# Optimization experiments

Measured on AMD Instinct MI355X. Metric: run time of the kernel, lower is better.

The kernel has to match this reference:

```python
import jax, jax.numpy as jnp
import numpy as np

ALPHA = 0.0005
BETA = 0.1
MARGIN = 100.0
GCN_WEIGHT = 0.1
EPS = 1e-8


def _bce(pred, tgt):
    # torch.nn.BCELoss with mean reduction (pred already in (0,1))
    return -jnp.mean(tgt * jnp.log(pred) + (1.0 - tgt) * jnp.log(1.0 - pred))


def _gcn_loss(nodes, labels, sample_idx):
    # nodes: [B, M, D], labels: [B, M] in {-1,0,1}, sample_idx: [B, S]
    n2 = jnp.sum(nodes * nodes, axis=-1)                               # [B, M]
    s_nodes = jnp.take_along_axis(nodes, sample_idx[:, :, None], axis=1)  # [B, S, D]
    s_lab = jnp.take_along_axis(labels, sample_idx, axis=1)            # [B, S]
    s2 = jnp.take_along_axis(n2, sample_idx, axis=1)                   # [B, S]
    cross = jnp.einsum('bsd,bmd->bsm', s_nodes, nodes)                 # [B, S, M]
    d2 = jnp.maximum(s2[:, :, None] + n2[:, None, :] - 2.0 * cross, 0.0)
    valid = labels >= 0
    same = (labels[:, None, :] == s_lab[:, :, None]) & valid[:, None, :]
    opp = (labels[:, None, :] != s_lab[:, :, None]) & valid[:, None, :]
    BIG = jnp.float32(1e30)
    # farthest same-label node, closest opposite-label node (L2 distance; sqrt is monotone)
    pos_idx = jnp.argmax(jnp.where(same, d2, -BIG), axis=-1)           # [B, S]
    neg_idx = jnp.argmin(jnp.where(opp, d2, BIG), axis=-1)             # [B, S]
    s_norm = jnp.sqrt(s2)

    def _cos(idx):
        dot = jnp.take_along_axis(cross, idx[:, :, None], axis=2)[..., 0]
        nb = jnp.sqrt(jnp.take_along_axis(n2, idx, axis=1))
        return dot / (jnp.maximum(s_norm, EPS) * jnp.maximum(nb, EPS))

    pos_loss = jnp.where(jnp.any(same, axis=-1), _cos(pos_idx), 0.0)
    neg_loss = jnp.where(jnp.any(opp, axis=-1), _cos(neg_idx), 0.0)
    return jnp.sum(pos_loss + neg_loss)


def setup_inputs() -> dict:
    key = jax.random.key(0)
    ks = jax.random.split(key, 10)
    B, T, D, C, M, S = 32, 750, 2048, 20, 750, 64
    score_act = jax.random.uniform(ks[0], (B, C)) * 0.98 + 0.01   # sigmoid-like probs in (0,1)
    score_bkg = jax.random.uniform(ks[1], (B, C)) * 0.98 + 0.01
    feat_act = jax.random.normal(ks[2], (B, T, D))
    feat_bkg = jax.random.normal(ks[3], (B, T, D))
    label = (jax.random.uniform(ks[4], (B, C)) < 0.3).astype(jnp.float32)
    label = label.at[:, 0].set(1.0)  # guarantee >=1 positive class per video
    gt = jax.random.uniform(ks[5], (B, T, C))
    cas = jax.random.normal(ks[6], (B, T, C))
    nodes = jax.random.normal(ks[7], (B, M, D))
    nodes_label = jax.random.randint(ks[8], (B, M), 0, 2)
    sample_idx = jax.random.randint(ks[9], (B, S), 0, M)
    return {'score_act': score_act, 'score_bkg': score_bkg, 'feat_act': feat_act,
            'feat_bkg': feat_bkg, 'label': label, 'gt': gt, 'cas': cas,
            'nodes': nodes, 'nodes_label': nodes_label, 'sample_idx': sample_idx}


def reference(score_act, score_bkg, feat_act, feat_bkg, label, gt, cas, nodes, nodes_label, sample_idx):
    label_n = label / jnp.sum(label, axis=1, keepdims=True)
    loss_cls = _bce(score_act, label_n)
    label_bkg = jnp.ones_like(label) / label.shape[1]
    loss_be = _bce(score_bkg, label_bkg)
    loss_act = jnp.maximum(MARGIN - jnp.linalg.norm(jnp.mean(feat_act, axis=1), axis=1), 0.0)
    loss_bkg = jnp.linalg.norm(jnp.mean(feat_bkg, axis=1), axis=1)
    loss_um = jnp.mean((loss_act + loss_bkg) ** 2)
    loss_gcn = GCN_WEIGHT * _gcn_loss(nodes, nodes_label, sample_idx)
    return loss_cls + ALPHA * loss_um + BETA * loss_be + loss_gcn
```

## Files before the change

kernel.cpp:

```cpp
#include <hip/hip_runtime.h>
#include <math.h>

#define BB 32
#define TT 750
#define DD 2048
#define CC 20
#define MM 750
#define SS 64
#define MT 64
#define NT 12
#define TSPLIT 8
#define TCH 94

#define GCN_BLOCKS (NT * BB)
#define FEAT_BLOCKS (2 * BB * TSPLIT * 2)
#define TOT_BLOCKS (GCN_BLOCKS + FEAT_BLOCKS + 1)

#define ALPHA_W 0.0005f
#define BETA_W 0.1f
#define MARGIN_W 100.0f
#define GCN_W 0.1f
#define EPS_V 1e-8f

#define WS_LOSS01 0
#define WS_N2ACT 16
#define WS_N2BKG 48
#define WS_GCNB 80
#define WS_S2 128
#define WS_CAND 4096
#define WS_COLSUM 200704

typedef __attribute__((ext_vector_type(8))) short bf16x8;
typedef __attribute__((ext_vector_type(4))) float f32x4;

__device__ __forceinline__ unsigned short f2bf(float f) {
  unsigned int u = __float_as_uint(f);
  return (unsigned short)((u + 0x7FFFu + ((u >> 16) & 1u)) >> 16);
}

__global__ __launch_bounds__(256, 3) void mega_kernel(
    const float* __restrict__ score_act, const float* __restrict__ score_bkg,
    const float* __restrict__ feat_act, const float* __restrict__ feat_bkg,
    const float* __restrict__ label, const float* __restrict__ nodes,
    const int* __restrict__ nlab, const int* __restrict__ sidx,
    float* __restrict__ ws) {
  int bx = blockIdx.x;
  int tid = threadIdx.x;
  int q11 = bx / 11, r11 = bx % 11;

  if (bx < TOT_BLOCKS - 1 && r11 < 3) {
    int idx = q11 * 3 + r11;
    int b = idx / NT, tile = idx % NT;

    __shared__ __align__(16) unsigned short sAh[64 * 64];
    __shared__ __align__(16) unsigned short sBh[64 * 64];
    __shared__ float sS2[SS];
    __shared__ float sN2[MT];
    __shared__ int sSlab[SS];
    __shared__ int sMlab[MT];

    if (tid < SS) {
      sSlab[tid] = nlab[b * MM + sidx[b * SS + tid]];
    } else if (tid < SS + MT) {
      int ml = tid - SS;
      int m = tile * MT + ml;
      sMlab[ml] = (m < MM) ? nlab[b * MM + m] : -2;
    }

    int r = tid >> 2, p = tid & 3;
    const float* aRow = nodes + ((size_t)b * MM + sidx[b * SS + r]) * DD;
    int mrow = tile * MT + r;
    bool bval = (mrow < MM);
    const float* bRow = nodes + ((size_t)b * MM + (bval ? mrow : 0)) * DD;

    int wslot[4];
#pragma unroll
    for (int j = 0; j < 4; ++j) {
      int u = p + 4 * j;
      wslot[j] = r * 64 + ((((u >> 1) ^ (r & 7)) << 1) + (u & 1)) * 4;
    }

    int lane = tid & 63, w = tid >> 6;
    int g = lane >> 4, c = lane & 15;

    float aSq = 0.f, bSq = 0.f;
    f32x4 acc[4];
#pragma unroll
    for (int f = 0; f < 4; ++f) acc[f] = (f32x4){0.f, 0.f, 0.f, 0.f};

    float4 pa[4], pb[4];
#pragma unroll
    for (int j = 0; j < 4; ++j) {
      int off = (p + 4 * j) * 4;
      pa[j] = *(const float4*)(aRow + off);
      pb[j] = *(const float4*)(bRow + off);
    }

    for (int ch = 0; ch < 32; ++ch) {
      __syncthreads();
#pragma unroll
      for (int j = 0; j < 4; ++j) {
        float4 v = pa[j];
        aSq += v.x * v.x + v.y * v.y + v.z * v.z + v.w * v.w;
        unsigned int lo = (unsigned int)f2bf(v.x) | ((unsigned int)f2bf(v.y) << 16);
        unsigned int hi = (unsigned int)f2bf(v.z) | ((unsigned int)f2bf(v.w) << 16);
        *(uint2*)&sAh[wslot[j]] = make_uint2(lo, hi);
        float4 t = pb[j];
        bSq += t.x * t.x + t.y * t.y + t.z * t.z + t.w * t.w;
        lo = (unsigned int)f2bf(t.x) | ((unsigned int)f2bf(t.y) << 16);
        hi = (unsigned int)f2bf(t.z) | ((unsigned int)f2bf(t.w) << 16);
        *(uint2*)&sBh[wslot[j]] = make_uint2(lo, hi);
      }
      __syncthreads();
      if (ch < 31) {
        const float* ap = aRow + (ch + 1) * 64;
        const float* bp = bRow + (ch + 1) * 64;
#pragma unroll
        for (int j = 0; j < 4; ++j) {
          int off = (p + 4 * j) * 4;
          pa[j] = *(const float4*)(ap + off);
          pb[j] = *(const float4*)(bp + off);
        }
      }
#pragma unroll
      for (int kk = 0; kk < 2; ++kk) {
        int su = kk * 4 + g;
        int arow = w * 16 + c;
        bf16x8 af = *(const bf16x8*)&sAh[arow * 64 + (su ^ (arow & 7)) * 8];
#pragma unroll
        for (int f = 0; f < 4; ++f) {
          int brow = f * 16 + c;
          bf16x8 bfr = *(const bf16x8*)&sBh[brow * 64 + (su ^ (brow & 7)) * 8];
          acc[f] = __builtin_amdgcn_mfma_f32_16x16x32_bf16(af, bfr, acc[f], 0, 0, 0);
        }
      }
    }

    aSq += __shfl_down(aSq, 2, 4);
    aSq += __shfl_down(aSq, 1, 4);
    bSq += __shfl_down(bSq, 2, 4);
    bSq += __shfl_down(bSq, 1, 4);
    if (p == 0) {
      sS2[r] = aSq;
      sN2[r] = bSq;
    }
    __syncthreads();

    if (tile == 0 && tid < SS) ws[WS_S2 + b * SS + tid] = sS2[tid];

#pragma unroll
    for (int reg = 0; reg < 4; ++reg) {
      int s = w * 16 + g * 4 + reg;
      int slab = sSlab[s];
      float s2v = sS2[s];
      float posD = -3.4e38f, posC = 0.f, posN = 0.f;
      int posI = -1;
      float negD = 3.4e38f, negC = 0.f, negN = 0.f;
      int negI = -1;
#pragma unroll
      for (int f = 0; f < 4; ++f) {
        int ml = f * 16 + c;
        int lab = sMlab[ml];
        float cv = acc[f][reg];
        float n2 = sN2[ml];
        float d2 = fmaxf(s2v + n2 - 2.f * cv, 0.f);
        if (lab >= 0 && lab == slab && (posI < 0 || d2 > posD)) {
          posD = d2; posI = tile * MT + ml; posC = cv; posN = n2;
        }
        if (lab >= 0 && lab != slab && (negI < 0 || d2 < negD)) {
          negD = d2; negI = tile * MT + ml; negC = cv; negN = n2;
        }
      }
#pragma unroll
      for (int off = 8; off; off >>= 1) {
        float oD = __shfl_down(posD, off, 16);
        int oI = __shfl_down(posI, off, 16);
        float oC = __shfl_down(posC, off, 16);
        float oN = __shfl_down(posN, off, 16);
        bool take = (oI >= 0) &&
                    (posI < 0 || oD > posD || (oD == posD && oI < posI));
        if (take) { posD = oD; posI = oI; posC = oC; posN = oN; }
        oD = __shfl_down(negD, off, 16);
        oI = __shfl_down(negI, off, 16);
        oC = __shfl_down(negC, off, 16);
        oN = __shfl_down(negN, off, 16);
        take = (oI >= 0) &&
               (negI < 0 || oD < negD || (oD == negD && oI < negI));
        if (take) { negD = oD; negI = oI; negC = oC; negN = oN; }
      }
      if (c == 0) {
        size_t base = (((size_t)b * SS + s) * NT + tile) * 8;
        *(float4*)&ws[WS_CAND + base] =
            make_float4(posD, __int_as_float(posI), posC, posN);
        *(float4*)&ws[WS_CAND + base + 4] =
            make_float4(negD, __int_as_float(negI), negC, negN);
      }
    }
  } else if (bx < TOT_BLOCKS - 1) {
    int idx = q11 * 8 + (r11 - 3);
    int tz = idx >> 9;
    int rem = idx & 511;
    int fb = rem >> 4;
    int sub = rem & 15;
    int blk = sub >> 1;
    int dh = sub & 1;
    const float* feat = tz ? feat_bkg : feat_act;
    int t0 = blk * TCH;
    int t1 = t0 + TCH < TT ? t0 + TCH : TT;
    const float* bp = feat + (size_t)fb * TT * DD + dh * 1024 + tid * 4;
    f32x4 a0 = {0.f, 0.f, 0.f, 0.f}, a1 = {0.f, 0.f, 0.f, 0.f};
    f32x4 a2 = {0.f, 0.f, 0.f, 0.f}, a3 = {0.f, 0.f, 0.f, 0.f};
    int t = t0;
    for (; t + 3 < t1; t += 4) {
      f32x4 v0 = __builtin_nontemporal_load((const f32x4*)(bp + (size_t)t * DD));
      f32x4 v1 =
          __builtin_nontemporal_load((const f32x4*)(bp + (size_t)(t + 1) * DD));
      f32x4 v2 =
          __builtin_nontemporal_load((const f32x4*)(bp + (size_t)(t + 2) * DD));
      f32x4 v3 =
          __builtin_nontemporal_load((const f32x4*)(bp + (size_t)(t + 3) * DD));
      a0 += v0;
      a1 += v1;
      a2 += v2;
      a3 += v3;
    }
    for (; t < t1; ++t)
      a0 += __builtin_nontemporal_load((const f32x4*)(bp + (size_t)t * DD));
    f32x4 rsum = (a0 + a2) + (a1 + a3);
    float* cs = ws + WS_COLSUM +
                ((size_t)(tz * BB + fb) * TSPLIT + blk) * DD + dh * 1024 +
                tid * 4;
    *(f32x4*)cs = rsum;
  } else {
    float vc = 0.f, vb = 0.f;
    for (int i = tid; i < BB * CC; i += 256) {
      int b = i / CC, c = i % CC;
      float rs = 0.f;
      for (int k = 0; k < CC; ++k) rs += label[b * CC + k];
      float ln = label[b * CC + c] / rs;
      float pa = score_act[i];
      vc += ln * logf(pa) + (1.f - ln) * logf(1.f - pa);
      float pb = score_bkg[i];
      const float tb = 1.f / (float)CC;
      vb += tb * logf(pb) + (1.f - tb) * logf(1.f - pb);
    }
    for (int off = 32; off; off >>= 1) {
      vc += __shfl_down(vc, off, 64);
      vb += __shfl_down(vb, off, 64);
    }
    __shared__ float rc[4], rb[4];
    if ((tid & 63) == 0) {
      rc[tid >> 6] = vc;
      rb[tid >> 6] = vb;
    }
    __syncthreads();
    if (tid == 0) {
      ws[WS_LOSS01] = -(rc[0] + rc[1] + rc[2] + rc[3]) / (float)(BB * CC);
      ws[WS_LOSS01 + 1] = -(rb[0] + rb[1] + rb[2] + rb[3]) / (float)(BB * CC);
    }
  }
}

__global__ __launch_bounds__(256) void tail_kernel(float* __restrict__ ws) {
  int bx = blockIdx.x, tid = threadIdx.x;
  if (bx < 64) {
    int tz = bx >> 5, fb = bx & 31;
    const float* cs = ws + WS_COLSUM + (size_t)(tz * BB + fb) * TSPLIT * DD;
    int d0 = tid * 8;
    float4 A0 = make_float4(0.f, 0.f, 0.f, 0.f);
    float4 A1 = make_float4(0.f, 0.f, 0.f, 0.f);
    for (int blk = 0; blk < TSPLIT; ++blk) {
      const float* pp = cs + blk * DD + d0;
      float4 u = *(const float4*)pp;
      float4 v = *(const float4*)(pp + 4);
      A0.x += u.x; A0.y += u.y; A0.z += u.z; A0.w += u.w;
      A1.x += v.x; A1.y += v.y; A1.z += v.z; A1.w += v.w;
    }
    const float inv = 1.f / (float)TT;
    float m0 = A0.x * inv, m1 = A0.y * inv, m2 = A0.z * inv, m3 = A0.w * inv;
    float m4 = A1.x * inv, m5 = A1.y * inv, m6 = A1.z * inv, m7 = A1.w * inv;
    float v = m0 * m0 + m1 * m1 + m2 * m2 + m3 * m3 +
              m4 * m4 + m5 * m5 + m6 * m6 + m7 * m7;
    for (int off = 32; off; off >>= 1) v += __shfl_down(v, off, 64);
    __shared__ float red[4];
    if ((tid & 63) == 0) red[tid >> 6] = v;
    __syncthreads();
    if (tid == 0)
      ws[(tz ? WS_N2BKG : WS_N2ACT) + fb] = red[0] + red[1] + red[2] + red[3];
  } else {
    int b = bx - 64;
    if (tid < SS) {
      const float* cb = ws + WS_CAND + ((size_t)b * SS + tid) * NT * 8;
      float posD = -3.4e38f, posC = 0.f, posN = 0.f;
      int posI = -1;
      float negD = 3.4e38f, negC = 0.f, negN = 0.f;
      int negI = -1;
      for (int t = 0; t < NT; ++t) {
        float4 pq = *(const float4*)&cb[t * 8];
        int oI = __float_as_int(pq.y);
        if (oI >= 0 && (posI < 0 || pq.x > posD || (pq.x == posD && oI < posI))) {
          posD = pq.x; posI = oI; posC = pq.z; posN = pq.w;
        }
        float4 qq = *(const float4*)&cb[t * 8 + 4];
        oI = __float_as_int(qq.y);
        if (oI >= 0 && (negI < 0 || qq.x < negD || (qq.x == negD && oI < negI))) {
          negD = qq.x; negI = oI; negC = qq.z; negN = qq.w;
        }
      }
      float snorm = sqrtf(ws[WS_S2 + b * SS + tid]);
      float sden = fmaxf(snorm, EPS_V);
      float pl = (posI >= 0) ? posC / (sden * fmaxf(sqrtf(posN), EPS_V)) : 0.f;
      float nl = (negI >= 0) ? negC / (sden * fmaxf(sqrtf(negN), EPS_V)) : 0.f;
      float v = pl + nl;
      for (int off = 32; off; off >>= 1) v += __shfl_down(v, off, 64);
      if (tid == 0) ws[WS_GCNB + b] = v;
    }
  }
}

__global__ void final_kernel(const float* __restrict__ ws,
                             float* __restrict__ out) {
  int tid = threadIdx.x;
  float um = 0.f, g = 0.f;
  if (tid < BB) {
    float la = fmaxf(MARGIN_W - sqrtf(ws[WS_N2ACT + tid]), 0.f);
    float lb = sqrtf(ws[WS_N2BKG + tid]);
    um = (la + lb) * (la + lb);
    g = ws[WS_GCNB + tid];
  }
  for (int off = 32; off; off >>= 1) {
    um += __shfl_down(um, off, 64);
    g += __shfl_down(g, off, 64);
  }
  if (tid == 0)
    out[0] = ws[WS_LOSS01] + BETA_W * ws[WS_LOSS01 + 1] +
             ALPHA_W * (um / (float)BB) + GCN_W * g;
}

extern "C" void kernel_launch(void* const* d_in, const int* in_sizes, int n_in,
                              void* d_out, int out_size, void* d_ws,
                              size_t ws_size, hipStream_t stream) {
  const float* score_act = (const float*)d_in[0];
  const float* score_bkg = (const float*)d_in[1];
  const float* feat_act = (const float*)d_in[2];
  const float* feat_bkg = (const float*)d_in[3];
  const float* label = (const float*)d_in[4];
  const float* nodes = (const float*)d_in[7];
  const int* nlab = (const int*)d_in[8];
  const int* sidx = (const int*)d_in[9];
  float* out = (float*)d_out;
  float* wsf = (float*)d_ws;

  mega_kernel<<<TOT_BLOCKS, 256, 0, stream>>>(
      score_act, score_bkg, feat_act, feat_bkg, label, nodes, nlab, sidx, wsf);
  tail_kernel<<<96, 256, 0, stream>>>(wsf);
  final_kernel<<<1, 64, 0, stream>>>(wsf, out);
}
```

Before: 135.1 us.

## Split fused mega kernel into separate feature-reduction and GCN kernels

After: 127.0 us. -5.9%, faster.

```diff
diff --git a/kernel.cpp b/kernel.cpp
--- a/kernel.cpp
+++ b/kernel.cpp
@@ -9,12 +9,9 @@
 #define SS 64
 #define MT 64
 #define NT 12
-#define TSPLIT 8
-#define TCH 94
-
-#define GCN_BLOCKS (NT * BB)
-#define FEAT_BLOCKS (2 * BB * TSPLIT * 2)
-#define TOT_BLOCKS (GCN_BLOCKS + FEAT_BLOCKS + 1)
+#define FSPLIT 16
+#define FROWS 47
+#define FUNITS (2 * BB * FSPLIT)
 
 #define ALPHA_W 0.0005f
 #define BETA_W 0.1f
@@ -38,19 +35,54 @@
   return (unsigned short)((u + 0x7FFFu + ((u >> 16) & 1u)) >> 16);
 }
 
-__global__ __launch_bounds__(256, 3) void mega_kernel(
+__global__ __launch_bounds__(512) void feat_kernel(
+    const float* __restrict__ feat_act, const float* __restrict__ feat_bkg,
+    float* __restrict__ ws) {
+  int u = blockIdx.x;
+  int tid = threadIdx.x;
+  int tz = u >> 9;
+  int rem = u & 511;
+  int fb = rem >> 4;
+  int sub = rem & 15;
+  const float* feat = tz ? feat_bkg : feat_act;
+  int t0 = sub * FROWS;
+  int t1 = t0 + FROWS < TT ? t0 + FROWS : TT;
+  const float* bp = feat + (size_t)fb * TT * DD + tid * 4;
+
+  f32x4 a0 = {0.f, 0.f, 0.f, 0.f}, a1 = {0.f, 0.f, 0.f, 0.f};
+  f32x4 a2 = {0.f, 0.f, 0.f, 0.f}, a3 = {0.f, 0.f, 0.f, 0.f};
+  int t = t0;
+  for (; t + 3 < t1; t += 4) {
+    f32x4 v0 = __builtin_nontemporal_load((const f32x4*)(bp + (size_t)t * DD));
+    f32x4 v1 =
+        __builtin_nontemporal_load((const f32x4*)(bp + (size_t)(t + 1) * DD));
+    f32x4 v2 =
+        __builtin_nontemporal_load((const f32x4*)(bp + (size_t)(t + 2) * DD));
+    f32x4 v3 =
+        __builtin_nontemporal_load((const f32x4*)(bp + (size_t)(t + 3) * DD));
+    a0 += v0;
+    a1 += v1;
+    a2 += v2;
+    a3 += v3;
+  }
+  for (; t < t1; ++t)
+    a0 += __builtin_nontemporal_load((const f32x4*)(bp + (size_t)t * DD));
+  f32x4 r = (a0 + a2) + (a1 + a3);
+  float* cs =
+      ws + WS_COLSUM + ((size_t)(tz * BB + fb) * FSPLIT + sub) * DD + tid * 4;
+  *(f32x4*)cs = r;
+}
+
+__global__ __launch_bounds__(256, 3) void gcn_kernel(
     const float* __restrict__ score_act, const float* __restrict__ score_bkg,
-    const float* __restrict__ feat_act, const float* __restrict__ feat_bkg,
     const float* __restrict__ label, const float* __restrict__ nodes,
     const int* __restrict__ nlab, const int* __restrict__ sidx,
     float* __restrict__ ws) {
   int bx = blockIdx.x;
   int tid = threadIdx.x;
-  int q11 = bx / 11, r11 = bx % 11;
-
-  if (bx < TOT_BLOCKS - 1 && r11 < 3) {
-    int idx = q11 * 3 + r11;
-    int b = idx / NT, tile = idx % NT;
+
+  if (bx < NT * BB) {
+    int b = bx / NT, tile = bx % NT;
 
     __shared__ __align__(16) unsigned short sAh[64 * 64];
     __shared__ __align__(16) unsigned short sBh[64 * 64];
@@ -196,41 +228,6 @@
             make_float4(negD, __int_as_float(negI), negC, negN);
       }
     }
-  } else if (bx < TOT_BLOCKS - 1) {
-    int idx = q11 * 8 + (r11 - 3);
-    int tz = idx >> 9;
-    int rem = idx & 511;
-    int fb = rem >> 4;
-    int sub = rem & 15;
-    int blk = sub >> 1;
-    int dh = sub & 1;
-    const float* feat = tz ? feat_bkg : feat_act;
-    int t0 = blk * TCH;
-    int t1 = t0 + TCH < TT ? t0 + TCH : TT;
-    const float* bp = feat + (size_t)fb * TT * DD + dh * 1024 + tid * 4;
-    f32x4 a0 = {0.f, 0.f, 0.f, 0.f}, a1 = {0.f, 0.f, 0.f, 0.f};
-    f32x4 a2 = {0.f, 0.f, 0.f, 0.f}, a3 = {0.f, 0.f, 0.f, 0.f};
-    int t = t0;
-    for (; t + 3 < t1; t += 4) {
-      f32x4 v0 = __builtin_nontemporal_load((const f32x4*)(bp + (size_t)t * DD));
-      f32x4 v1 =
-          __builtin_nontemporal_load((const f32x4*)(bp + (size_t)(t + 1) * DD));
-      f32x4 v2 =
-          __builtin_nontemporal_load((const f32x4*)(bp + (size_t)(t + 2) * DD));
-      f32x4 v3 =
-          __builtin_nontemporal_load((const f32x4*)(bp + (size_t)(t + 3) * DD));
-      a0 += v0;
-      a1 += v1;
-      a2 += v2;
-      a3 += v3;
-    }
-    for (; t < t1; ++t)
-      a0 += __builtin_nontemporal_load((const f32x4*)(bp + (size_t)t * DD));
-    f32x4 rsum = (a0 + a2) + (a1 + a3);
-    float* cs = ws + WS_COLSUM +
-                ((size_t)(tz * BB + fb) * TSPLIT + blk) * DD + dh * 1024 +
-                tid * 4;
-    *(f32x4*)cs = rsum;
   } else {
     float vc = 0.f, vb = 0.f;
     for (int i = tid; i < BB * CC; i += 256) {
@@ -265,11 +262,11 @@
   int bx = blockIdx.x, tid = threadIdx.x;
   if (bx < 64) {
     int tz = bx >> 5, fb = bx & 31;
-    const float* cs = ws + WS_COLSUM + (size_t)(tz * BB + fb) * TSPLIT * DD;
+    const float* cs = ws + WS_COLSUM + (size_t)(tz * BB + fb) * FSPLIT * DD;
     int d0 = tid * 8;
     float4 A0 = make_float4(0.f, 0.f, 0.f, 0.f);
     float4 A1 = make_float4(0.f, 0.f, 0.f, 0.f);
-    for (int blk = 0; blk < TSPLIT; ++blk) {
+    for (int blk = 0; blk < FSPLIT; ++blk) {
       const float* pp = cs + blk * DD + d0;
       float4 u = *(const float4*)pp;
       float4 v = *(const float4*)(pp + 4);
@@ -351,8 +348,9 @@
   float* out = (float*)d_out;
   float* wsf = (float*)d_ws;
 
-  mega_kernel<<<TOT_BLOCKS, 256, 0, stream>>>(
-      score_act, score_bkg, feat_act, feat_bkg, label, nodes, nlab, sidx, wsf);
+  feat_kernel<<<FUNITS, 512, 0, stream>>>(feat_act, feat_bkg, wsf);
+  gcn_kernel<<<NT * BB + 1, 256, 0, stream>>>(score_act, score_bkg, label,
+                                              nodes, nlab, sidx, wsf);
   tail_kernel<<<96, 256, 0, stream>>>(wsf);
   final_kernel<<<1, 64, 0, stream>>>(wsf, out);
 }
```
